# Kernel optimization log

Hardware: AMD Instinct MI355X
Metric: run time of the kernel (lower is better)

## Reference

```python
import jax, jax.numpy as jnp
import numpy as np
from jax import lax

B, N = 4096, 2048  # batteries, Euler steps (throughput has N+1 columns)
D_IN, D_HID = 5, 10


def setup_inputs() -> dict:
    key = jax.random.key(0)
    ks = jax.random.split(key, 10)
    # monotone throughput so Euler step sizes h are positive and realistic
    thr = jnp.cumsum(jax.random.uniform(ks[0], (B, N + 1), jnp.float32) * 0.01, axis=1)
    return {
        "throughput": thr,
        "DOD": jax.random.uniform(ks[1], (1, B), jnp.float32),
        "V_av": jax.random.uniform(ks[2], (1, B), jnp.float32) * 0.8 + 3.2,
        "C_0": jax.random.uniform(ks[3], (1, B), jnp.float32) * 0.2 + 0.9,
        "R_0": jax.random.uniform(ks[4], (1, B), jnp.float32) * 0.05 + 0.01,
        "W1": jax.random.normal(ks[5], (D_HID, D_IN), jnp.float32) / np.sqrt(D_IN),
        "b1": jax.random.normal(ks[6], (D_HID,), jnp.float32) * 0.01,
        "W2": jax.random.normal(ks[7], (D_IN, D_HID), jnp.float32) / np.sqrt(D_HID),
        "b2": jax.random.normal(ks[8], (D_IN,), jnp.float32) * 0.01,
        "n": N,
    }


def reference(throughput, DOD, V_av, C_0, R_0, W1, b1, W2, b2, n):
    # initial state per battery: [thr_0, DOD, V_av, C_0, R_0] -> [B, 5]
    init = jnp.concatenate(
        [throughput[:, 0:1], DOD.T, V_av.T, C_0.T, R_0.T], axis=1
    )

    def f(y):  # tiny MLP: Linear(5,10)-Tanh-Linear(10,5)
        return jnp.tanh(y @ W1.T + b1) @ W2.T + b2

    thr_next = throughput[:, 1 : n + 1]              # [B, n]
    hs = thr_next - throughput[:, 0:n]               # [B, n] Euler step sizes

    def step(state, xs):
        h, t = xs                                    # each [B]
        y_new = state + h[:, None] * f(state)        # Euler step on full state
        # pin feature 0 to current throughput, reset features 1:3 to initial
        new_state = jnp.concatenate(
            [t[:, None], state[:, 1:3], y_new[:, 3:5]], axis=1
        )
        return new_state, new_state[:, 3:5]

    _, outs = lax.scan(step, init, (hs.T, thr_next.T))  # outs: [n, B, 2]
    traj = jnp.concatenate([init[None, :, 3:5], outs], axis=0)  # [n+1, B, 2]
    return jnp.transpose(traj, (1, 0, 2))            # [B, n+1, 2]
```

## Files before the change

kernel.cpp:

```cpp
#include <hip/hip_runtime.h>

typedef float v2f __attribute__((ext_vector_type(2)));

__device__ __forceinline__ float scan64(float d) {
    d += __int_as_float(__builtin_amdgcn_update_dpp(0, __float_as_int(d), 0x111, 0xF, 0xF, true));
    d += __int_as_float(__builtin_amdgcn_update_dpp(0, __float_as_int(d), 0x112, 0xF, 0xF, true));
    d += __int_as_float(__builtin_amdgcn_update_dpp(0, __float_as_int(d), 0x114, 0xF, 0xF, true));
    d += __int_as_float(__builtin_amdgcn_update_dpp(0, __float_as_int(d), 0x118, 0xF, 0xF, true));
    d += __int_as_float(__builtin_amdgcn_update_dpp(0, __float_as_int(d), 0x142, 0xA, 0xF, true));
    d += __int_as_float(__builtin_amdgcn_update_dpp(0, __float_as_int(d), 0x143, 0xC, 0xF, true));
    return d;
}

__device__ __forceinline__ float rdl63(float v) {
    return __int_as_float(__builtin_amdgcn_readlane(__float_as_int(v), 63));
}

__global__ __launch_bounds__(64, 4) void ode_wf256x4st(
    const float* __restrict__ thr,
    const float* __restrict__ DOD,
    const float* __restrict__ Vav,
    const float* __restrict__ C0,
    const float* __restrict__ R0,
    const float* __restrict__ W1,
    const float* __restrict__ b1,
    const float* __restrict__ W2,
    const float* __restrict__ b2,
    float* __restrict__ out,
    int B, int N)
{
    const int j   = threadIdx.x & 63;
    const int row = blockIdx.x;
    if (row >= B) return;

    const float k2  = 2.0f * 1.4426950408889634f;
    const float ln2 = 0.6931471805599453f;
    const float dod = DOD[row], vav = Vav[row];

    v2f bw[5], w0k[5], w3k[5], w4k[5], wa[5], wb[5];
    float c3 = b2[3], c4 = b2[4];
#pragma unroll
    for (int i = 0; i < 5; ++i) {
#pragma unroll
        for (int p = 0; p < 2; ++p) {
            int h = i + 5 * p;
            float a0 = W1[h * 5 + 0];
            float a1 = W1[h * 5 + 1];
            float a2 = W1[h * 5 + 2];
            float a3 = W1[h * 5 + 3];
            float a4 = W1[h * 5 + 4];
            bw[i][p]  = k2 * (b1[h] + a1 * dod + a2 * vav);
            w0k[i][p] = k2 * a0;
            w3k[i][p] = k2 * a3;
            w4k[i][p] = k2 * a4;
            float v3 = W2[30 + h];
            float v4 = W2[40 + h];
            c3 += v3; c4 += v4;
            wa[i][p] = -2.0f * v3;
            wb[i][p] = -2.0f * v4;
        }
    }

    float Y3 = C0[row], Y4 = R0[row];
    const float* trp = thr + (size_t)row * (size_t)(N + 1);
    float2* orow = (float2*)(out + (size_t)row * (size_t)(N + 1) * 2);
    const bool alignA = ((row & 1) == 0);
    if (!alignA && j == 0) orow[0] = make_float2(Y3, Y4);

    float tc[5], tn[5], tbc, tbn;
#pragma unroll
    for (int k = 0; k < 5; ++k) tc[k] = trp[min(4 * j + k, N)];
    tbc = trp[0];
#pragma unroll
    for (int k = 0; k < 5; ++k) tn[k] = trp[min(256 + 4 * j + k, N)];
    tbn = trp[min(256, N)];

    float F3p, F4p;
    {
        v2f Fa = {c3, 0.f}, Fb = {c4, 0.f};
#pragma unroll
        for (int i = 0; i < 5; ++i) {
            v2f x = w3k[i] * Y3 + (w4k[i] * Y4 + (w0k[i] * tbc + bw[i]));
            v2f e; e.x = __builtin_amdgcn_exp2f(x.x); e.y = __builtin_amdgcn_exp2f(x.y);
            v2f A = e + 1.0f;
            v2f s; s.x = __builtin_amdgcn_rcpf(A.x); s.y = __builtin_amdgcn_rcpf(A.y);
            Fa += wa[i] * s;
            Fb += wb[i] * s;
        }
        F3p = Fa.x + Fa.y; F4p = Fb.x + Fb.y;
    }
    float dF3 = 0.f, dF4 = 0.f;

    const int nblk = (N + 255) >> 8;
    const int nSt  = N >> 8;

    for (int g = 0; g < nblk; ++g) {
        const int base = g << 8;

        const int pf = base + 512;
        float tf[5], tbf;
#pragma unroll
        for (int k = 0; k < 5; ++k) tf[k] = trp[min(pf + 4 * j + k, N)];
        tbf = trp[min(pf, N)];

        const float h0 = tc[1] - tc[0];
        const float h1 = tc[2] - tc[1];
        const float h2 = tc[3] - tc[2];
        const float h3 = tc[4] - tc[3];

        float z3[4], z4[4];
#pragma unroll
        for (int k = 0; k < 4; ++k) {
            float dt = tc[k] - tbc;
            z3[k] = fmaf(dt, fmaf(0.5f * dt, dF3, F3p), Y3);
            z4[k] = fmaf(dt, fmaf(0.5f * dt, dF4, F4p), Y4);
        }

        v2f tq[5];
        float F30, F40;
        {
            v2f Fa = {c3, 0.f}, Fb = {c4, 0.f};
#pragma unroll
            for (int i = 0; i < 5; ++i) {
                v2f x = w3k[i] * z3[0] + (w4k[i] * z4[0] + (w0k[i] * tc[0] + bw[i]));
                v2f e; e.x = __builtin_amdgcn_exp2f(x.x);
                       e.y = __builtin_amdgcn_exp2f(x.y);
                v2f A = e + 1.0f;
                v2f s; s.x = __builtin_amdgcn_rcpf(A.x);
                       s.y = __builtin_amdgcn_rcpf(A.y);
                tq[i] = s;
                Fa += wa[i] * s;
                Fb += wb[i] * s;
            }
            F30 = Fa.x + Fa.y; F40 = Fb.x + Fb.y;
        }
#pragma unroll
        for (int i = 0; i < 5; ++i) tq[i] = tq[i] - tq[i] * tq[i];

        float K3a, K4a, Kta, K3b, K4b, Ktb;
        {
            v2f a3 = {0.f,0.f}, a4 = {0.f,0.f}, at = {0.f,0.f};
            v2f b3 = {0.f,0.f}, b4 = {0.f,0.f}, bt = {0.f,0.f};
#pragma unroll
            for (int i = 0; i < 5; ++i) {
                v2f ma = wa[i] * tq[i];
                v2f mb = wb[i] * tq[i];
                a3 += ma * w3k[i]; a4 += ma * w4k[i]; at += ma * w0k[i];
                b3 += mb * w3k[i]; b4 += mb * w4k[i]; bt += mb * w0k[i];
            }
            K3a = ln2 * (a3.x + a3.y); K4a = ln2 * (a4.x + a4.y);
            Kta = ln2 * (at.x + at.y);
            K3b = ln2 * (b3.x + b3.y); K4b = ln2 * (b4.x + b4.y);
            Ktb = ln2 * (bt.x + bt.y);
        }

        float F3v[4], F4v[4];
        F3v[0] = F30; F4v[0] = F40;
#pragma unroll
        for (int k = 1; k < 4; ++k) {
            float D3 = z3[k] - z3[0];
            float D4 = z4[k] - z4[0];
            float Dt = tc[k] - tc[0];
            F3v[k] = F30 - fmaf(K3a, D3, fmaf(K4a, D4, Kta * Dt));
            F4v[k] = F40 - fmaf(K3b, D3, fmaf(K4b, D4, Ktb * Dt));
        }

        float d3 = fmaf(h0, F3v[0], fmaf(h1, F3v[1], fmaf(h2, F3v[2], h3 * F3v[3])));
        float d4 = fmaf(h0, F4v[0], fmaf(h1, F4v[1], fmaf(h2, F4v[2], h3 * F4v[3])));
        float S3 = scan64(d3);
        float S4 = scan64(d4);

        float dm3, dm4;
        {
            float cb3 = Y3 + (S3 - d3), cb4 = Y4 + (S4 - d4);
            float a1 = h0 * F3v[0];
            float a2 = fmaf(h1, F3v[1], a1);
            float a3 = fmaf(h2, F3v[2], a2);
            float b1_ = h0 * F4v[0];
            float b2_ = fmaf(h1, F4v[1], b1_);
            float b3_ = fmaf(h2, F4v[2], b2_);
            float e0 = cb3 - z3[0];
            float e1 = (cb3 + a1) - z3[1];
            float e2 = (cb3 + a2) - z3[2];
            float e3 = (cb3 + a3) - z3[3];
            dm3 = fmaf(h0, e0, h1 * e1) + fmaf(h2, e2, h3 * e3);
            float f0 = cb4 - z4[0];
            float f1 = (cb4 + b1_) - z4[1];
            float f2 = (cb4 + b2_) - z4[2];
            float f3 = (cb4 + b3_) - z4[3];
            dm4 = fmaf(h0, f0, h1 * f1) + fmaf(h2, f2, h3 * f3);
        }

        float d3p = d3 - fmaf(K3a, dm3, K4a * dm4);
        float d4p = d4 - fmaf(K3b, dm3, K4b * dm4);
        float S3p = scan64(d3p);
        float S4p = scan64(d4p);

        float o3 = Y3 + S3p, o4 = Y4 + S4p;
        float w23 = fmaf(-h3, F3v[3], o3), w24 = fmaf(-h3, F4v[3], o4);
        float w13 = fmaf(-h2, F3v[2], w23), w14 = fmaf(-h2, F4v[2], w24);
        float w03 = fmaf(-h1, F3v[1], w13), w04 = fmaf(-h1, F4v[1], w14);
        const int p0 = base + 4 * j;
        if (g < nSt) {
            if (alignA) {
                float b3 = Y3 + (S3p - d3p), b4 = Y4 + (S4p - d4p);
                float4* dst = (float4*)(orow + p0);
                float4 v0 = {b3, b4, w03, w04};
                float4 v1 = {w13, w14, w23, w24};
                dst[0] = v0;
                dst[1] = v1;
                if (p0 + 4 == N) orow[N] = make_float2(o3, o4);
            } else {
                float4* dst = (float4*)(orow + p0 + 1);
                float4 v0 = {w03, w04, w13, w14};
                float4 v1 = {w23, w24, o3, o4};
                dst[0] = v0;
                dst[1] = v1;
            }
        } else {
            if (alignA && j == 0) orow[base] = make_float2(Y3, Y4);
            if (p0 + 3 < N) orow[p0 + 4] = make_float2(o3, o4);
            if (p0 + 2 < N) orow[p0 + 3] = make_float2(w23, w24);
            if (p0 + 1 < N) orow[p0 + 2] = make_float2(w13, w14);
            if (p0 < N)     orow[p0 + 1] = make_float2(w03, w04);
        }

        float F3n = rdl63(F3v[3]);
        float F4n = rdl63(F4v[3]);
        Y3 += rdl63(S3p);
        Y4 += rdl63(S4p);
        float span = tbn - tbc;
        float inv = (span > 0.f) ? __builtin_amdgcn_rcpf(span) : 0.f;
        dF3 = (F3n - F3p) * inv;
        dF4 = (F4n - F4p) * inv;
        F3p = F3n; F4p = F4n;

#pragma unroll
        for (int k = 0; k < 5; ++k) { tc[k] = tn[k]; tn[k] = tf[k]; }
        tbc = tbn; tbn = tbf;
    }
}

extern "C" void kernel_launch(void* const* d_in, const int* in_sizes, int n_in,
                              void* d_out, int out_size, void* d_ws, size_t ws_size,
                              hipStream_t stream) {
    const float* thr = (const float*)d_in[0];
    const float* DOD = (const float*)d_in[1];
    const float* Vav = (const float*)d_in[2];
    const float* C0  = (const float*)d_in[3];
    const float* R0  = (const float*)d_in[4];
    const float* W1  = (const float*)d_in[5];
    const float* b1  = (const float*)d_in[6];
    const float* W2  = (const float*)d_in[7];
    const float* b2  = (const float*)d_in[8];
    float* out = (float*)d_out;

    int B = in_sizes[1];
    int N = in_sizes[0] / B - 1;

    dim3 block(64);
    dim3 grid(B);
    ode_wf256x4st<<<grid, block, 0, stream>>>(thr, DOD, Vav, C0, R0,
                                              W1, b1, W2, b2, out, B, N);
}
```

Measured before the change: 29.98 us.

## Stage throughput tiles through LDS with double-buffered direct global-to-LDS loads

Replaces the per-lane register prefetch of throughput values with `global_load_lds` transfers into a two-slot shared-memory buffer. Each lane issues coalesced unit-stride loads, and the compute loop reads its five strided values back from LDS. The aim is cleaner global access and lower register pressure from the prefetch arrays. In exchange, prefetch distance drops from two blocks to one, the top-of-loop `s_waitcnt vmcnt(0)` may also wait on outstanding output stores, and the stride-4 LDS reads can cause bank conflicts.

```diff
diff --git a/kernel.cpp b/kernel.cpp
--- a/kernel.cpp
+++ b/kernel.cpp
@@ -16,7 +16,7 @@
     return __int_as_float(__builtin_amdgcn_readlane(__float_as_int(v), 63));
 }
 
-__global__ __launch_bounds__(64, 4) void ode_wf256x4st(
+__global__ __launch_bounds__(64, 4) void ode_wf256lds(
     const float* __restrict__ thr,
     const float* __restrict__ DOD,
     const float* __restrict__ Vav,
@@ -32,6 +32,8 @@
     const int j   = threadIdx.x & 63;
     const int row = blockIdx.x;
     if (row >= B) return;
+
+    __shared__ float tl[2][320];
 
     const float k2  = 2.0f * 1.4426950408889634f;
     const float ln2 = 0.6931471805599453f;
@@ -67,20 +69,21 @@
     const bool alignA = ((row & 1) == 0);
     if (!alignA && j == 0) orow[0] = make_float2(Y3, Y4);
 
-    float tc[5], tn[5], tbc, tbn;
-#pragma unroll
-    for (int k = 0; k < 5; ++k) tc[k] = trp[min(4 * j + k, N)];
-    tbc = trp[0];
-#pragma unroll
-    for (int k = 0; k < 5; ++k) tn[k] = trp[min(256 + 4 * j + k, N)];
-    tbn = trp[min(256, N)];
-
+#pragma unroll
+    for (int i = 0; i < 5; ++i) {
+        int idx = min(i * 64 + j, N);
+        __builtin_amdgcn_global_load_lds(
+            (const __attribute__((address_space(1))) float*)(trp + idx),
+            (__attribute__((address_space(3))) float*)&tl[0][i * 64], 4, 0, 0);
+    }
+
+    float tb0 = trp[0];
     float F3p, F4p;
     {
         v2f Fa = {c3, 0.f}, Fb = {c4, 0.f};
 #pragma unroll
         for (int i = 0; i < 5; ++i) {
-            v2f x = w3k[i] * Y3 + (w4k[i] * Y4 + (w0k[i] * tbc + bw[i]));
+            v2f x = w3k[i] * Y3 + (w4k[i] * Y4 + (w0k[i] * tb0 + bw[i]));
             v2f e; e.x = __builtin_amdgcn_exp2f(x.x); e.y = __builtin_amdgcn_exp2f(x.y);
             v2f A = e + 1.0f;
             v2f s; s.x = __builtin_amdgcn_rcpf(A.x); s.y = __builtin_amdgcn_rcpf(A.y);
@@ -93,15 +96,28 @@
 
     const int nblk = (N + 255) >> 8;
     const int nSt  = N >> 8;
+    int cur = 0;
 
     for (int g = 0; g < nblk; ++g) {
         const int base = g << 8;
-
-        const int pf = base + 512;
-        float tf[5], tbf;
-#pragma unroll
-        for (int k = 0; k < 5; ++k) tf[k] = trp[min(pf + 4 * j + k, N)];
-        tbf = trp[min(pf, N)];
+        const int nb = base + 256;
+        const int nxt = cur ^ 1;
+
+        asm volatile("s_waitcnt vmcnt(0)" ::: "memory");
+
+        float tc[5];
+#pragma unroll
+        for (int k = 0; k < 5; ++k) tc[k] = tl[cur][4 * j + k];
+        const float tbc = tl[cur][0];
+        const float tbn = tl[cur][256];
+
+#pragma unroll
+        for (int i = 0; i < 5; ++i) {
+            int idx = min(nb + i * 64 + j, N);
+            __builtin_amdgcn_global_load_lds(
+                (const __attribute__((address_space(1))) float*)(trp + idx),
+                (__attribute__((address_space(3))) float*)&tl[nxt][i * 64], 4, 0, 0);
+        }
 
         const float h0 = tc[1] - tc[0];
         const float h1 = tc[2] - tc[1];
@@ -235,9 +251,7 @@
         dF4 = (F4n - F4p) * inv;
         F3p = F3n; F4p = F4n;
 
-#pragma unroll
-        for (int k = 0; k < 5; ++k) { tc[k] = tn[k]; tn[k] = tf[k]; }
-        tbc = tbn; tbn = tbf;
+        cur = nxt;
     }
 }
 
@@ -260,6 +274,6 @@
 
     dim3 block(64);
     dim3 grid(B);
-    ode_wf256x4st<<<grid, block, 0, stream>>>(thr, DOD, Vav, C0, R0,
-                                              W1, b1, W2, b2, out, B, N);
-}
+    ode_wf256lds<<<grid, block, 0, stream>>>(thr, DOD, Vav, C0, R0,
+                                             W1, b1, W2, b2, out, B, N);
+}
```

Result: no change. 30.13 us (+0.5%).
